# Performance work log

Hardware: AMD Instinct MI355X
Metric: run time of the kernel (lower is better)

Reference implementation:

```python
import jax, jax.numpy as jnp
import numpy as np

B, N, D, H = 2, 2048, 1024, 16
HD = D // H
SCALE = HD ** -0.5


def setup_inputs() -> dict:
    key = jax.random.key(0)
    ks = jax.random.split(key, 5)
    s = D ** -0.5  # keep activations well-scaled like torch Linear init
    return {
        "x": jax.random.normal(ks[0], (B, N, D), jnp.float32),
        "Wq": jax.random.normal(ks[1], (D, D), jnp.float32) * s,
        "bq": jnp.zeros((D,), jnp.float32),
        "Wk": jax.random.normal(ks[2], (D, D), jnp.float32) * s,
        "bk": jnp.zeros((D,), jnp.float32),
        "Wv": jax.random.normal(ks[3], (D, D), jnp.float32) * s,
        "bv": jnp.zeros((D,), jnp.float32),
        "Wo": jax.random.normal(ks[4], (D, D), jnp.float32) * s,
        "bo": jnp.zeros((D,), jnp.float32),
    }


def reference(x, Wq, bq, Wk, bk, Wv, bv, Wo, bo):
    # projections: [B,N,D] -> [B,H,N,HD]
    def split_heads(t):
        return t.reshape(B, N, H, HD).transpose(0, 2, 1, 3)

    q = split_heads(x @ Wq + bq)
    k = split_heads(x @ Wk + bk)
    v = split_heads(x @ Wv + bv)
    # eager attention: explicit [B,H,N,N] scores, matching the torch module
    attn = jnp.einsum("bhnd,bhmd->bhnm", q, k) * SCALE
    attn = jax.nn.softmax(attn, axis=-1)
    out = jnp.einsum("bhnm,bhmd->bhnd", attn, v)
    out = out.transpose(0, 2, 1, 3).reshape(B, N, D)
    return out @ Wo + bo
```

## Files before the change

### kernel.cpp

```cpp
#include <hip/hip_runtime.h>
#include <hip/hip_bf16.h>

typedef __attribute__((ext_vector_type(8))) short bf16x8;
typedef __attribute__((ext_vector_type(4))) float f32x4;
typedef __attribute__((ext_vector_type(4))) unsigned short us4;
typedef __attribute__((ext_vector_type(8))) unsigned short us8;
typedef unsigned short u16;

#define NB 2
#define NSEQ 2048
#define DM 1024
#define NH 16
#define HD 64
#define NTOK (NB*NSEQ)
#define QK_SCALE (0.125f * 1.4426950408889634f)

__device__ __forceinline__ u16 f2b(float f) {
  __hip_bfloat16 h = __float2bfloat16(f);
  return __builtin_bit_cast(u16, h);
}

__device__ __forceinline__ unsigned pkbf(float a, float b) {
  return (unsigned)f2b(a) | ((unsigned)f2b(b) << 16);
}

__device__ __forceinline__ void gload16(const void* g, void* l) {
  __builtin_amdgcn_global_load_lds((__attribute__((address_space(1))) void*)g,
                                   (__attribute__((address_space(3))) void*)l, 16, 0, 0);
}

__global__ __launch_bounds__(256) void k_convx(const float* __restrict__ x, u16* __restrict__ xb) {
  const int idx = (blockIdx.x * 256 + threadIdx.x) * 8;
  const float4 v0 = *(const float4*)(x + idx);
  const float4 v1 = *(const float4*)(x + idx + 4);
  us8 o;
  o[0]=f2b(v0.x); o[1]=f2b(v0.y); o[2]=f2b(v0.z); o[3]=f2b(v0.w);
  o[4]=f2b(v1.x); o[5]=f2b(v1.y); o[6]=f2b(v1.z); o[7]=f2b(v1.w);
  *(us8*)(xb + idx) = o;
}

__global__ __launch_bounds__(256) void k_twt(const float* __restrict__ W, u16* __restrict__ WT) {
  __shared__ float tile[64][68];
  const int n0 = blockIdx.x * 64, k0 = blockIdx.y * 64;
  const int tr = threadIdx.x >> 4, tc = (threadIdx.x & 15) * 4;
#pragma unroll
  for (int rr = 0; rr < 4; ++rr) {
    const int r = rr * 16 + tr;
    *(float4*)&tile[r][tc] = *(const float4*)&W[(size_t)(k0 + r) * DM + n0 + tc];
  }
  __syncthreads();
#pragma unroll
  for (int rr = 0; rr < 4; ++rr) {
    const int nr = rr * 16 + tr;
    us4 o;
#pragma unroll
    for (int e = 0; e < 4; ++e) o[e] = f2b(tile[tc + e][nr]);
    *(us4*)&WT[(size_t)(n0 + nr) * DM + k0 + tc] = o;
  }
}

template<int MODE>
__global__ __launch_bounds__(256) void k_gemm(
    const u16* __restrict__ A, const u16* __restrict__ A1,
    const u16* __restrict__ Bt,
    const float* __restrict__ bias, const float* __restrict__ bias1,
    void* __restrict__ out0, void* __restrict__ out1,
    float scale0, float scale1)
{
  const u16* Ap = A; const float* bp = bias; void* outp = out0; float scale = scale0;
  if (MODE == 0 && blockIdx.z == 1) { Ap = A1; bp = bias1; outp = out1; scale = scale1; }

  __shared__ char smem[64 * 1024];
  const int tid = threadIdx.x, lane = tid & 63, wv = tid >> 6;
  const int li = lane & 15, g = lane >> 4;
  const int wi = wv >> 1, wj = wv & 1;
  const int i0 = blockIdx.y * 128, j0 = blockIdx.x * 128;

  f32x4 acc[4][4];
#pragma unroll
  for (int a = 0; a < 4; ++a)
#pragma unroll
    for (int b = 0; b < 4; ++b) acc[a][b] = f32x4{0.f, 0.f, 0.f, 0.f};

  auto stage = [&](int kt, int buf) {
#pragma unroll
    for (int c = 0; c < 4; ++c) {
      const int lg = c * 256 + tid;
      const int r = lg >> 3, ch = (lg & 7) ^ (r & 7);
      gload16(Ap + (size_t)(i0 + r) * 1024 + kt * 64 + ch * 8,
              smem + buf * 32768 + (c * 256 + wv * 64) * 16);
      gload16(Bt + (size_t)(j0 + r) * 1024 + kt * 64 + ch * 8,
              smem + buf * 32768 + 16384 + (c * 256 + wv * 64) * 16);
    }
  };

  stage(0, 0);

  for (int kt = 0; kt < 16; ++kt) {
    __syncthreads();
    if (kt + 1 < 16) stage(kt + 1, (kt + 1) & 1);
    const char* As = smem + (kt & 1) * 32768;
    const char* Bs = As + 16384;
#pragma unroll
    for (int ks = 0; ks < 2; ++ks) {
      bf16x8 af[4], bfr[4];
#pragma unroll
      for (int it = 0; it < 4; ++it) {
        const int ri = 64 * wi + 16 * it + li;
        af[it] = *(const bf16x8*)(As + ri * 128 + ((ks * 64 + g * 16) ^ ((ri & 7) << 4)));
        const int rj = 64 * wj + 16 * it + li;
        bfr[it] = *(const bf16x8*)(Bs + rj * 128 + ((ks * 64 + g * 16) ^ ((rj & 7) << 4)));
      }
#pragma unroll
      for (int it = 0; it < 4; ++it)
#pragma unroll
        for (int jt = 0; jt < 4; ++jt)
          acc[it][jt] = __builtin_amdgcn_mfma_f32_16x16x32_bf16(af[it], bfr[jt], acc[it][jt], 0, 0, 0);
    }
  }

#pragma unroll
  for (int it = 0; it < 4; ++it) {
    const int ib = i0 + 64 * wi + 16 * it + 4 * g;
    f32x4 b4;
    if constexpr (MODE != 1) b4 = *(const f32x4*)(bp + ib);
#pragma unroll
    for (int jt = 0; jt < 4; ++jt) {
      const int j = j0 + 64 * wj + 16 * jt + li;
      f32x4 v = acc[it][jt];
      if constexpr (MODE == 1) {
        const float bj = bp[j];
        v[0] += bj; v[1] += bj; v[2] += bj; v[3] += bj;
      } else {
        v += b4;
      }
      if constexpr (MODE == 0) {
        v *= scale;
        us4 pk; pk[0]=f2b(v[0]); pk[1]=f2b(v[1]); pk[2]=f2b(v[2]); pk[3]=f2b(v[3]);
        *(us4*)((u16*)outp + (size_t)j * 1024 + ib) = pk;
      } else if constexpr (MODE == 1) {
        us4 pk; pk[0]=f2b(v[0]); pk[1]=f2b(v[1]); pk[2]=f2b(v[2]); pk[3]=f2b(v[3]);
        const size_t addr = ((size_t)(ib >> 11) * 1024 + j) * 2048 + (ib & 2047);
        *(us4*)((u16*)outp + addr) = pk;
      } else {
        *(f32x4*)((float*)outp + (size_t)j * 1024 + ib) = v;
      }
    }
  }
}

__global__ __launch_bounds__(256) void k_attn(const u16* __restrict__ Q, const u16* __restrict__ K,
                                              const u16* __restrict__ Vt, u16* __restrict__ O)
{
  __shared__ char smem[40 * 1024];
  const int tid = threadIdx.x, lane = tid & 63, w = tid >> 6;
  const int li = lane & 15, g = lane >> 4;
  const int bh = blockIdx.y, b = bh >> 4, h = bh & 15;
  const int n0 = blockIdx.x * 64;
  const size_t tokbase = (size_t)b * NSEQ;
  const int iq = 16 * w + li;
  const int nq = n0 + iq;

  bf16x8 qf[2];
#pragma unroll
  for (int ks = 0; ks < 2; ++ks)
    qf[ks] = *(const bf16x8*)(Q + (tokbase + nq) * 1024 + h * 64 + 32 * ks + 8 * g);

  bf16x8 ones;
#pragma unroll
  for (int e = 0; e < 8; ++e) ones[e] = (short)0x3F80;

  f32x4 oacc[4];
#pragma unroll
  for (int dt = 0; dt < 4; ++dt) oacc[dt] = f32x4{0.f, 0.f, 0.f, 0.f};
  f32x4 ls = f32x4{0.f, 0.f, 0.f, 0.f};

  const u16* Kb = K + tokbase * 1024 + h * 64;
  const u16* Vb = Vt + (size_t)bh * 64 * 2048;

  auto stage = [&](int t, int buf) {
    const int jn = t * 64;
#pragma unroll
    for (int c = 0; c < 2; ++c) {
      const int lg = c * 256 + tid;
      const int r = lg >> 3, ch = (lg & 7) ^ (r & 7);
      gload16(Kb + (size_t)(jn + r) * 1024 + ch * 8, smem + buf * 8192 + (c * 256 + w * 64) * 16);
      gload16(Vb + (size_t)r * 2048 + jn + ch * 8, smem + 16384 + buf * 8192 + (c * 256 + w * 64) * 16);
    }
  };

  stage(0, 0);

  for (int t = 0; t < 32; ++t) {
    __syncthreads();
    if (t + 1 < 32) stage(t + 1, (t + 1) & 1);
    const char* Ks = smem + (t & 1) * 8192;
    const char* Vs = smem + 16384 + (t & 1) * 8192;

    f32x4 s[4];
#pragma unroll
    for (int jt = 0; jt < 4; ++jt) s[jt] = f32x4{0.f, 0.f, 0.f, 0.f};
#pragma unroll
    for (int ks = 0; ks < 2; ++ks) {
#pragma unroll
      for (int jt = 0; jt < 4; ++jt) {
        const int rj = 16 * jt + li;
        bf16x8 a = *(const bf16x8*)(Ks + rj * 128 + ((ks * 64 + g * 16) ^ ((rj & 7) << 4)));
        s[jt] = __builtin_amdgcn_mfma_f32_16x16x32_bf16(a, qf[ks], s[jt], 0, 0, 0);
      }
    }

#pragma unroll
    for (int jt = 0; jt < 4; ++jt) {
      uint2 pk;
      pk.x = pkbf(exp2f(s[jt][0]), exp2f(s[jt][1]));
      pk.y = pkbf(exp2f(s[jt][2]), exp2f(s[jt][3]));
      *(uint2*)(smem + 32768 + iq * 128 + ((32 * jt + 8 * g) ^ ((iq & 7) << 4))) = pk;
    }

#pragma unroll
    for (int ks = 0; ks < 2; ++ks) {
      const int kb = ks * 64 + g * 16;
      bf16x8 bpv = *(const bf16x8*)(smem + 32768 + iq * 128 + (kb ^ ((iq & 7) << 4)));
      ls = __builtin_amdgcn_mfma_f32_16x16x32_bf16(ones, bpv, ls, 0, 0, 0);
#pragma unroll
      for (int dt = 0; dt < 4; ++dt) {
        const int rd = 16 * dt + li;
        bf16x8 av = *(const bf16x8*)(Vs + rd * 128 + (kb ^ ((rd & 7) << 4)));
        oacc[dt] = __builtin_amdgcn_mfma_f32_16x16x32_bf16(av, bpv, oacc[dt], 0, 0, 0);
      }
    }
  }

  const float inv = 1.f / ls[0];
#pragma unroll
  for (int dt = 0; dt < 4; ++dt) {
    us4 pk;
#pragma unroll
    for (int e = 0; e < 4; ++e) pk[e] = f2b(oacc[dt][e] * inv);
    *(us4*)(O + (tokbase + nq) * 1024 + h * 64 + 16 * dt + 4 * g) = pk;
  }
}

extern "C" void kernel_launch(void* const* d_in, const int* in_sizes, int n_in,
                              void* d_out, int out_size, void* d_ws, size_t ws_size,
                              hipStream_t stream) {
  const float* x  = (const float*)d_in[0];
  const float* Wq = (const float*)d_in[1];
  const float* bq = (const float*)d_in[2];
  const float* Wk = (const float*)d_in[3];
  const float* bk = (const float*)d_in[4];
  const float* Wv = (const float*)d_in[5];
  const float* bv = (const float*)d_in[6];
  const float* Wo = (const float*)d_in[7];
  const float* bo = (const float*)d_in[8];

  char* ws = (char*)d_ws;
  u16* xb  = (u16*)(ws);
  u16* WqT = (u16*)(ws + (8  << 20));
  u16* WkT = (u16*)(ws + (10 << 20));
  u16* WvT = (u16*)(ws + (12 << 20));
  u16* WoT = (u16*)(ws + (14 << 20));
  u16* Qb  = (u16*)(ws + (16 << 20));
  u16* Kb  = (u16*)(ws + (24 << 20));
  u16* Vtb = (u16*)(ws + (32 << 20));
  u16* Ob  = (u16*)(ws + (40 << 20));

  k_convx<<<2048, 256, 0, stream>>>(x, xb);
  k_twt<<<dim3(16, 16), 256, 0, stream>>>(Wq, WqT);
  k_twt<<<dim3(16, 16), 256, 0, stream>>>(Wk, WkT);
  k_twt<<<dim3(16, 16), 256, 0, stream>>>(Wv, WvT);
  k_twt<<<dim3(16, 16), 256, 0, stream>>>(Wo, WoT);

  k_gemm<0><<<dim3(32, 8, 2), 256, 0, stream>>>(WqT, WkT, xb, bq, bk, Qb, Kb, QK_SCALE, 1.0f);
  k_gemm<1><<<dim3(8, 32, 1), 256, 0, stream>>>(xb, nullptr, WvT, bv, nullptr, Vtb, nullptr, 1.0f, 1.0f);

  k_attn<<<dim3(32, 32), 256, 0, stream>>>(Qb, Kb, Vtb, Ob);

  k_gemm<2><<<dim3(32, 8, 1), 256, 0, stream>>>(WoT, nullptr, Ob, bo, nullptr, d_out, nullptr, 1.0f, 1.0f);
}
```

Measured before the change: 143.0 us.

## Process 128 query rows per attention block and merge weight transpose launches

```diff
diff --git a/kernel.cpp b/kernel.cpp
--- a/kernel.cpp
+++ b/kernel.cpp
@@ -39,7 +39,12 @@
   *(us8*)(xb + idx) = o;
 }
 
-__global__ __launch_bounds__(256) void k_twt(const float* __restrict__ W, u16* __restrict__ WT) {
+__global__ __launch_bounds__(256) void k_twt4(const float* __restrict__ W0, const float* __restrict__ W1,
+                                              const float* __restrict__ W2, const float* __restrict__ W3,
+                                              u16* __restrict__ T0, u16* __restrict__ T1,
+                                              u16* __restrict__ T2, u16* __restrict__ T3) {
+  const float* W = (blockIdx.z == 0) ? W0 : (blockIdx.z == 1) ? W1 : (blockIdx.z == 2) ? W2 : W3;
+  u16* WT = (blockIdx.z == 0) ? T0 : (blockIdx.z == 1) ? T1 : (blockIdx.z == 2) ? T2 : T3;
   __shared__ float tile[64][68];
   const int n0 = blockIdx.x * 64, k0 = blockIdx.y * 64;
   const int tr = threadIdx.x >> 4, tc = (threadIdx.x & 15) * 4;
@@ -149,31 +154,34 @@
   }
 }
 
-__global__ __launch_bounds__(256) void k_attn(const u16* __restrict__ Q, const u16* __restrict__ K,
-                                              const u16* __restrict__ Vt, u16* __restrict__ O)
+__global__ __launch_bounds__(256, 2) void k_attn(const u16* __restrict__ Q, const u16* __restrict__ K,
+                                                 const u16* __restrict__ Vt, u16* __restrict__ O)
 {
-  __shared__ char smem[40 * 1024];
+  __shared__ char smem[48 * 1024];
   const int tid = threadIdx.x, lane = tid & 63, w = tid >> 6;
   const int li = lane & 15, g = lane >> 4;
   const int bh = blockIdx.y, b = bh >> 4, h = bh & 15;
-  const int n0 = blockIdx.x * 64;
+  const int n0 = blockIdx.x * 128;
   const size_t tokbase = (size_t)b * NSEQ;
   const int iq = 16 * w + li;
-  const int nq = n0 + iq;
-
-  bf16x8 qf[2];
-#pragma unroll
-  for (int ks = 0; ks < 2; ++ks)
-    qf[ks] = *(const bf16x8*)(Q + (tokbase + nq) * 1024 + h * 64 + 32 * ks + 8 * g);
+
+  bf16x8 qf[2][2];
+#pragma unroll
+  for (int grp = 0; grp < 2; ++grp)
+#pragma unroll
+    for (int ks = 0; ks < 2; ++ks)
+      qf[grp][ks] = *(const bf16x8*)(Q + (tokbase + n0 + 64 * grp + iq) * 1024 + h * 64 + 32 * ks + 8 * g);
 
   bf16x8 ones;
 #pragma unroll
   for (int e = 0; e < 8; ++e) ones[e] = (short)0x3F80;
 
-  f32x4 oacc[4];
-#pragma unroll
-  for (int dt = 0; dt < 4; ++dt) oacc[dt] = f32x4{0.f, 0.f, 0.f, 0.f};
-  f32x4 ls = f32x4{0.f, 0.f, 0.f, 0.f};
+  f32x4 oacc[2][4];
+#pragma unroll
+  for (int grp = 0; grp < 2; ++grp)
+#pragma unroll
+    for (int dt = 0; dt < 4; ++dt) oacc[grp][dt] = f32x4{0.f, 0.f, 0.f, 0.f};
+  f32x4 ls[2] = {f32x4{0.f,0.f,0.f,0.f}, f32x4{0.f,0.f,0.f,0.f}};
 
   const u16* Kb = K + tokbase * 1024 + h * 64;
   const u16* Vb = Vt + (size_t)bh * 64 * 2048;
@@ -189,56 +197,77 @@
     }
   };
 
-  stage(0, 0);
-
-  for (int t = 0; t < 32; ++t) {
+  auto tilebody = [&](int t, int buf) {
     __syncthreads();
-    if (t + 1 < 32) stage(t + 1, (t + 1) & 1);
-    const char* Ks = smem + (t & 1) * 8192;
-    const char* Vs = smem + 16384 + (t & 1) * 8192;
-
-    f32x4 s[4];
-#pragma unroll
-    for (int jt = 0; jt < 4; ++jt) s[jt] = f32x4{0.f, 0.f, 0.f, 0.f};
+    if (t + 1 < 32) stage(t + 1, buf ^ 1);
+    const char* Ks = smem + buf * 8192;
+    const char* Vs = smem + 16384 + buf * 8192;
+
+    f32x4 s[2][4];
+#pragma unroll
+    for (int grp = 0; grp < 2; ++grp)
+#pragma unroll
+      for (int jt = 0; jt < 4; ++jt) s[grp][jt] = f32x4{0.f, 0.f, 0.f, 0.f};
 #pragma unroll
     for (int ks = 0; ks < 2; ++ks) {
 #pragma unroll
       for (int jt = 0; jt < 4; ++jt) {
         const int rj = 16 * jt + li;
         bf16x8 a = *(const bf16x8*)(Ks + rj * 128 + ((ks * 64 + g * 16) ^ ((rj & 7) << 4)));
-        s[jt] = __builtin_amdgcn_mfma_f32_16x16x32_bf16(a, qf[ks], s[jt], 0, 0, 0);
-      }
-    }
-
-#pragma unroll
-    for (int jt = 0; jt < 4; ++jt) {
-      uint2 pk;
-      pk.x = pkbf(exp2f(s[jt][0]), exp2f(s[jt][1]));
-      pk.y = pkbf(exp2f(s[jt][2]), exp2f(s[jt][3]));
-      *(uint2*)(smem + 32768 + iq * 128 + ((32 * jt + 8 * g) ^ ((iq & 7) << 4))) = pk;
+        s[0][jt] = __builtin_amdgcn_mfma_f32_16x16x32_bf16(a, qf[0][ks], s[0][jt], 0, 0, 0);
+        s[1][jt] = __builtin_amdgcn_mfma_f32_16x16x32_bf16(a, qf[1][ks], s[1][jt], 0, 0, 0);
+      }
+    }
+
+#pragma unroll
+    for (int grp = 0; grp < 2; ++grp) {
+      const int row = iq + 64 * grp;
+      char* Pr = smem + 32768 + row * 128;
+      const int swz = (row & 7) << 4;
+#pragma unroll
+      for (int jt = 0; jt < 4; ++jt) {
+        uint2 pk;
+        pk.x = pkbf(exp2f(s[grp][jt][0]), exp2f(s[grp][jt][1]));
+        pk.y = pkbf(exp2f(s[grp][jt][2]), exp2f(s[grp][jt][3]));
+        *(uint2*)(Pr + ((32 * jt + 8 * g) ^ swz)) = pk;
+      }
     }
 
 #pragma unroll
     for (int ks = 0; ks < 2; ++ks) {
       const int kb = ks * 64 + g * 16;
-      bf16x8 bpv = *(const bf16x8*)(smem + 32768 + iq * 128 + (kb ^ ((iq & 7) << 4)));
-      ls = __builtin_amdgcn_mfma_f32_16x16x32_bf16(ones, bpv, ls, 0, 0, 0);
+      bf16x8 bpv0 = *(const bf16x8*)(smem + 32768 + iq * 128 + (kb ^ ((iq & 7) << 4)));
+      bf16x8 bpv1 = *(const bf16x8*)(smem + 32768 + (iq + 64) * 128 + (kb ^ ((iq & 7) << 4)));
+      ls[0] = __builtin_amdgcn_mfma_f32_16x16x32_bf16(ones, bpv0, ls[0], 0, 0, 0);
+      ls[1] = __builtin_amdgcn_mfma_f32_16x16x32_bf16(ones, bpv1, ls[1], 0, 0, 0);
 #pragma unroll
       for (int dt = 0; dt < 4; ++dt) {
         const int rd = 16 * dt + li;
         bf16x8 av = *(const bf16x8*)(Vs + rd * 128 + (kb ^ ((rd & 7) << 4)));
-        oacc[dt] = __builtin_amdgcn_mfma_f32_16x16x32_bf16(av, bpv, oacc[dt], 0, 0, 0);
-      }
-    }
-  }
-
-  const float inv = 1.f / ls[0];
-#pragma unroll
-  for (int dt = 0; dt < 4; ++dt) {
-    us4 pk;
-#pragma unroll
-    for (int e = 0; e < 4; ++e) pk[e] = f2b(oacc[dt][e] * inv);
-    *(us4*)(O + (tokbase + nq) * 1024 + h * 64 + 16 * dt + 4 * g) = pk;
+        oacc[0][dt] = __builtin_amdgcn_mfma_f32_16x16x32_bf16(av, bpv0, oacc[0][dt], 0, 0, 0);
+        oacc[1][dt] = __builtin_amdgcn_mfma_f32_16x16x32_bf16(av, bpv1, oacc[1][dt], 0, 0, 0);
+      }
+    }
+  };
+
+  stage(0, 0);
+#pragma unroll 1
+  for (int tt = 0; tt < 16; ++tt) {
+    tilebody(2 * tt, 0);
+    tilebody(2 * tt + 1, 1);
+  }
+
+#pragma unroll
+  for (int grp = 0; grp < 2; ++grp) {
+    const float inv = 1.f / ls[grp][0];
+    const size_t obase = (tokbase + n0 + 64 * grp + iq) * 1024 + h * 64;
+#pragma unroll
+    for (int dt = 0; dt < 4; ++dt) {
+      us4 pk;
+#pragma unroll
+      for (int e = 0; e < 4; ++e) pk[e] = f2b(oacc[grp][dt][e] * inv);
+      *(us4*)(O + obase + 16 * dt + 4 * g) = pk;
+    }
   }
 }
 
@@ -267,15 +296,12 @@
   u16* Ob  = (u16*)(ws + (40 << 20));
 
   k_convx<<<2048, 256, 0, stream>>>(x, xb);
-  k_twt<<<dim3(16, 16), 256, 0, stream>>>(Wq, WqT);
-  k_twt<<<dim3(16, 16), 256, 0, stream>>>(Wk, WkT);
-  k_twt<<<dim3(16, 16), 256, 0, stream>>>(Wv, WvT);
-  k_twt<<<dim3(16, 16), 256, 0, stream>>>(Wo, WoT);
+  k_twt4<<<dim3(16, 16, 4), 256, 0, stream>>>(Wq, Wk, Wv, Wo, WqT, WkT, WvT, WoT);
 
   k_gemm<0><<<dim3(32, 8, 2), 256, 0, stream>>>(WqT, WkT, xb, bq, bk, Qb, Kb, QK_SCALE, 1.0f);
   k_gemm<1><<<dim3(8, 32, 1), 256, 0, stream>>>(xb, nullptr, WvT, bv, nullptr, Vtb, nullptr, 1.0f, 1.0f);
 
-  k_attn<<<dim3(32, 32), 256, 0, stream>>>(Qb, Kb, Vtb, Ob);
+  k_attn<<<dim3(16, 32), 256, 0, stream>>>(Qb, Kb, Vtb, Ob);
 
   k_gemm<2><<<dim3(32, 8, 1), 256, 0, stream>>>(WoT, nullptr, Ob, bo, nullptr, d_out, nullptr, 1.0f, 1.0f);
 }
```

Measured after the change: 131.1 us. 1.09x faster.
